# Kernel tuning notes

Hardware: AMD Instinct MI355X
Metric: run time of the kernel (lower is better)

Reference implementation:

```python
import jax, jax.numpy as jnp
import numpy as np

VOCAB, EMB, HID, B, S = 32000, 512, 512, 64, 1024


def setup_inputs() -> dict:
    key = jax.random.key(0)
    ks = jax.random.split(key, 9)
    x = jax.random.randint(ks[0], (B, S), 0, VOCAB)
    lengths = jax.random.randint(ks[1], (B,), 1, S + 1)
    # embedding table; padding_idx=0 row is zero-initialized in torch
    emb_table = jax.random.normal(ks[2], (VOCAB, EMB), dtype=jnp.float32) * 0.02
    emb_table = emb_table.at[0].set(0.0)
    sc_e = 1.0 / np.sqrt(EMB)
    sc_h = 1.0 / np.sqrt(HID)
    W_ih0 = jax.random.uniform(ks[3], (EMB, HID), jnp.float32, -sc_e, sc_e)
    b0 = jax.random.uniform(ks[4], (HID,), jnp.float32, -sc_e, sc_e)
    W_hh0 = jax.random.uniform(ks[5], (HID, HID), jnp.float32, -sc_h, sc_h)
    W_ih1 = jax.random.uniform(ks[6], (HID, HID), jnp.float32, -sc_h, sc_h)
    b1 = jax.random.uniform(ks[7], (HID,), jnp.float32, -sc_h, sc_h)
    W_hh1 = jax.random.uniform(ks[8], (HID, HID), jnp.float32, -sc_h, sc_h)
    return {"x": x, "lengths": lengths, "emb_table": emb_table,
            "W_ih0": W_ih0, "b0": b0, "W_hh0": W_hh0,
            "W_ih1": W_ih1, "b1": b1, "W_hh1": W_hh1}


def reference(x, lengths, emb_table, W_ih0, b0, W_hh0, W_ih1, b1, W_hh1):
    # eval mode: dropout is identity
    emb = emb_table[x]                    # [B, S, E]
    emb_t = jnp.transpose(emb, (1, 0, 2))  # [S, B, E] for scan over time
    h0_init = jnp.zeros((x.shape[0], HID), emb.dtype)
    h1_init = jnp.zeros((x.shape[0], HID), emb.dtype)

    def step(carry, x_t):
        h0, h1 = carry
        h0 = jnp.tanh(x_t @ W_ih0 + b0 + h0 @ W_hh0)
        h1 = jnp.tanh(h0 @ W_ih1 + b1 + h1 @ W_hh1)
        return (h0, h1), h1

    (h0, h1), outs = jax.lax.scan(step, (h0_init, h1_init), emb_t)
    outputs = jnp.transpose(outs, (1, 0, 2))   # [B, S, H]
    hidden = jnp.stack([h0, h1], axis=0)       # [num_layers, B, H]
    return outputs, hidden
```

## Files before the change

kernel.cpp:

```cpp
#include <hip/hip_runtime.h>

#define S_LEN 1024
#define BATCH 64
#define HIDDEN 512
#define NGROUP 4
#define NBLK 32
#define COLS_PER_BLK 16
#define GRID_CAND 512
#define TRY_CAP (1 << 20)

typedef __attribute__((ext_vector_type(8))) short short8;
typedef __attribute__((ext_vector_type(4))) float f32x4;
typedef __attribute__((ext_vector_type(4))) unsigned int u32x4;

__device__ __forceinline__ unsigned short f2bf(float x) {
  unsigned u = __builtin_bit_cast(unsigned, x);
  u += 0x7fffu + ((u >> 16) & 1u);
  return (unsigned short)(u >> 16);
}
__device__ __forceinline__ float bf2f(unsigned short h) {
  unsigned u = ((unsigned)h) << 16;
  return __builtin_bit_cast(float, u);
}

#define HOFF(p, kc, l) ((((p) * 16 + (kc)) * 64 + (l)) * 8)

__global__ void k_init(unsigned* __restrict__ ws, int* __restrict__ hbufs) {
  int i = blockIdx.x * blockDim.x + threadIdx.x;
  if (i < 4096) ws[i] = 0u;
  for (int k = i; k < 131072; k += gridDim.x * blockDim.x) hbufs[k] = 0;
}

__launch_bounds__(256, 1)
__global__ void k_rnn(const int* __restrict__ x, const float* __restrict__ emb,
                      const float* __restrict__ Wih0, const float* __restrict__ b0,
                      const float* __restrict__ Whh0, const float* __restrict__ Wih1,
                      const float* __restrict__ b1, const float* __restrict__ Whh1,
                      float* __restrict__ out, unsigned* __restrict__ ws_u,
                      short* __restrict__ hbase) {
  __shared__ short wlds[8 * 16 * 64 * 8];
  __shared__ __align__(16) short stage0[2][32][8];
  __shared__ __align__(16) short stage1[2][32][8];
  __shared__ float accx[3][8][68];
  __shared__ int slot_sh, grp_sh;

  if (threadIdx.x == 0) {
    unsigned xcc;
    asm volatile("s_getreg_b32 %0, hwreg(HW_REG_XCC_ID)" : "=s"(xcc));
    int s = -1;
    if (xcc < NGROUP)
      s = (int)__hip_atomic_fetch_add(ws_u + 2048 + xcc * 16, 1u,
                                      __ATOMIC_RELAXED, __HIP_MEMORY_SCOPE_AGENT);
    slot_sh = s; grp_sh = (int)xcc;
  }
  __syncthreads();
  const int slot = slot_sh, grp = grp_sh;
  if ((unsigned)slot >= NBLK) return;

  const int tid  = threadIdx.x;
  const int wid  = tid >> 6;
  const int lane = tid & 63;
  const int col0 = slot * COLS_PER_BLK;

  {
    const float* Wm[4] = {Wih0, Whh0, Wih1, Whh1};
    const int c = col0 + (lane & 15);
    #pragma unroll
    for (int m = 0; m < 4; ++m) {
      const float* W = Wm[m];
      for (int kc = wid; kc < 16; kc += 4) {
        const int k0 = kc * 32 + (lane >> 4) * 8;
        const int basei = (kc * 64 + lane) * 8;
        #pragma unroll
        for (int j = 0; j < 8; ++j) {
          float v = W[(size_t)(k0 + j) * HIDDEN + c];
          unsigned short vh = f2bf(v);
          wlds[(m * 2    ) * 8192 + basei + j] = (short)vh;
          wlds[(m * 2 + 1) * 8192 + basei + j] = (short)f2bf(v - bf2f(vh));
        }
      }
    }
  }
  __syncthreads();

  short* gh    = hbase + grp * 65536;
  short* h0_hi = gh;
  short* h0_lo = gh + 16384;
  short* h1_hi = gh + 32768;
  short* h1_lo = gh + 49152;

  const int row0  = grp * 16;
  const int arow  = row0 + (lane & 15);
  const int kgo   = (lane >> 4) * 8;
  const int ccol  = col0 + (lane & 15);
  const int drow0 = (lane >> 4) * 4;
  const float bc0 = b0[ccol];
  const float bc1 = b1[ccol];

  const int skc   = col0 >> 5;
  const int sub0  = (slot & 1) * 2;
  const int sel2  = (lane & 15) >> 3;
  const int sjj   = lane & 7;

  float* out_seq = out;
  float* hidden  = out + (size_t)BATCH * S_LEN * HIDDEN;

  unsigned* gflags = ws_u + grp * 512;
  unsigned*       myflag = gflags + slot * 16;
  const unsigned* pollp  = gflags + (lane & 31) * 16;

  short8 ea_reg[4];
  #define LOAD_EA(t) do {                                                   \
    const int xr_ = x[arow * S_LEN + (t)];                                  \
    const float* erow_ = emb + (size_t)xr_ * HIDDEN;                        \
    _Pragma("unroll")                                                       \
    for (int k2 = 0; k2 < 4; ++k2) {                                        \
      const float4* ep_ = (const float4*)(erow_ + (wid * 4 + k2) * 32 + kgo); \
      float4 e0_ = ep_[0], e1_ = ep_[1];                                    \
      short8 ea_;                                                           \
      ea_[0] = (short)f2bf(e0_.x); ea_[1] = (short)f2bf(e0_.y);             \
      ea_[2] = (short)f2bf(e0_.z); ea_[3] = (short)f2bf(e0_.w);             \
      ea_[4] = (short)f2bf(e1_.x); ea_[5] = (short)f2bf(e1_.y);             \
      ea_[6] = (short)f2bf(e1_.z); ea_[7] = (short)f2bf(e1_.w);             \
      ea_reg[k2] = ea_;                                                     \
    } } while (0)

  LOAD_EA(0);

  for (int i = 0; i <= S_LEN; ++i) {
    const int p = i & 1;
    const int q = p ^ 1;
    const bool doL0 = (i < S_LEN);
    const bool doL1 = (i >= 1);

    f32x4 aA0 = {0.f, 0.f, 0.f, 0.f};
    f32x4 aA1 = {0.f, 0.f, 0.f, 0.f};
    f32x4 aB0 = {0.f, 0.f, 0.f, 0.f};
    f32x4 aB1 = {0.f, 0.f, 0.f, 0.f};
    #pragma unroll
    for (int k2 = 0; k2 < 4; ++k2) {
      const int kc = wid * 4 + k2;
      const int o0 = HOFF(q, kc, lane);
      const int o1 = HOFF(p, kc, lane);
      short8 ah = *(const short8*)(h0_hi + o0);
      short8 al = *(const short8*)(h0_lo + o0);
      short8 ch = *(const short8*)(h1_hi + o1);
      short8 cl = *(const short8*)(h1_lo + o1);
      const int fb = (kc * 64 + lane) * 8;
      if (doL0) {
        short8 w0h = *(const short8*)&wlds[0 * 8192 + fb];
        short8 w0l = *(const short8*)&wlds[1 * 8192 + fb];
        short8 g0h = *(const short8*)&wlds[2 * 8192 + fb];
        short8 g0l = *(const short8*)&wlds[3 * 8192 + fb];
        f32x4& ac = (k2 & 1) ? aA1 : aA0;
        ac = __builtin_amdgcn_mfma_f32_16x16x32_bf16(ea_reg[k2], w0h, ac, 0, 0, 0);
        ac = __builtin_amdgcn_mfma_f32_16x16x32_bf16(ea_reg[k2], w0l, ac, 0, 0, 0);
        ac = __builtin_amdgcn_mfma_f32_16x16x32_bf16(ah, g0h, ac, 0, 0, 0);
        ac = __builtin_amdgcn_mfma_f32_16x16x32_bf16(ah, g0l, ac, 0, 0, 0);
        ac = __builtin_amdgcn_mfma_f32_16x16x32_bf16(al, g0h, ac, 0, 0, 0);
      }
      if (doL1) {
        short8 w1h = *(const short8*)&wlds[4 * 8192 + fb];
        short8 w1l = *(const short8*)&wlds[5 * 8192 + fb];
        short8 g1h = *(const short8*)&wlds[6 * 8192 + fb];
        short8 g1l = *(const short8*)&wlds[7 * 8192 + fb];
        f32x4& bcx = (k2 & 1) ? aB1 : aB0;
        bcx = __builtin_amdgcn_mfma_f32_16x16x32_bf16(ah, w1h, bcx, 0, 0, 0);
        bcx = __builtin_amdgcn_mfma_f32_16x16x32_bf16(ah, w1l, bcx, 0, 0, 0);
        bcx = __builtin_amdgcn_mfma_f32_16x16x32_bf16(al, w1h, bcx, 0, 0, 0);
        bcx = __builtin_amdgcn_mfma_f32_16x16x32_bf16(ch, g1h, bcx, 0, 0, 0);
        bcx = __builtin_amdgcn_mfma_f32_16x16x32_bf16(ch, g1l, bcx, 0, 0, 0);
        bcx = __builtin_amdgcn_mfma_f32_16x16x32_bf16(cl, g1h, bcx, 0, 0, 0);
      }
    }

    if (wid) {
      #pragma unroll
      for (int j = 0; j < 4; ++j) {
        accx[wid - 1][j    ][lane] = aA0[j] + aA1[j];
        accx[wid - 1][4 + j][lane] = aB0[j] + aB1[j];
      }
    }
    __syncthreads();

    if (wid == 0) {
      float hv0[4], hv1[4];
      if (doL0) {
        #pragma unroll
        for (int j = 0; j < 4; ++j) {
          float s = aA0[j] + aA1[j] + accx[0][j][lane] + accx[1][j][lane]
                  + accx[2][j][lane] + bc0;
          hv0[j] = tanhf(s);
          unsigned short hi = f2bf(hv0[j]);
          unsigned short lo = f2bf(hv0[j] - bf2f(hi));
          stage0[0][drow0 + j + 16 * sel2][sjj] = (short)hi;
          stage0[1][drow0 + j + 16 * sel2][sjj] = (short)lo;
        }
      }
      if (doL1) {
        #pragma unroll
        for (int j = 0; j < 4; ++j) {
          float s = aB0[j] + aB1[j] + accx[0][4 + j][lane] + accx[1][4 + j][lane]
                  + accx[2][4 + j][lane] + bc1;
          hv1[j] = tanhf(s);
          unsigned short hi = f2bf(hv1[j]);
          unsigned short lo = f2bf(hv1[j] - bf2f(hi));
          stage1[0][drow0 + j + 16 * sel2][sjj] = (short)hi;
          stage1[1][drow0 + j + 16 * sel2][sjj] = (short)lo;
        }
      }
      asm volatile("s_waitcnt lgkmcnt(0)" ::: "memory");
      const int l2 = lane & 31, sel = lane >> 5;
      if (doL0) {
        u32x4 v = *(const u32x4*)&stage0[sel][l2][0];
        short* dst = (sel ? h0_lo : h0_hi) + HOFF(p, skc, sub0 * 16 + l2);
        *(u32x4*)dst = v;
      }
      if (doL1) {
        u32x4 v = *(const u32x4*)&stage1[sel][l2][0];
        short* dst = (sel ? h1_lo : h1_hi) + HOFF(q, skc, sub0 * 16 + l2);
        *(u32x4*)dst = v;
      }
      if (doL1) {
        const int t = i - 1;
        #pragma unroll
        for (int j = 0; j < 4; ++j)
          out_seq[(size_t)(row0 + drow0 + j) * S_LEN * HIDDEN
                  + (size_t)t * HIDDEN + ccol] = hv1[j];
        if (i == S_LEN) {
          #pragma unroll
          for (int j = 0; j < 4; ++j)
            hidden[32768 + (row0 + drow0 + j) * HIDDEN + ccol] = hv1[j];
        }
      }
      if (doL0 && i == S_LEN - 1) {
        #pragma unroll
        for (int j = 0; j < 4; ++j)
          hidden[(row0 + drow0 + j) * HIDDEN + ccol] = hv0[j];
      }
    }

    if (i < S_LEN) {
      if (wid == 0) {
        asm volatile("s_waitcnt vmcnt(0)" ::: "memory");
        if (lane == 0)
          __hip_atomic_store(myflag, (unsigned)(i + 1),
                             __ATOMIC_RELAXED, __HIP_MEMORY_SCOPE_AGENT);
      }
      if (i + 1 < S_LEN) LOAD_EA(i + 1);
      __builtin_amdgcn_sched_barrier(0);
      if (wid == 0) {
        int tries = 0;
        for (;;) {
          unsigned f = __hip_atomic_load(pollp, __ATOMIC_RELAXED,
                                         __HIP_MEMORY_SCOPE_AGENT);
          if (__all((int)(f > (unsigned)i))) break;
          if (++tries > TRY_CAP) break;
        }
      }
      __syncthreads();
    }
  }
  #undef LOAD_EA
}

extern "C" void kernel_launch(void* const* d_in, const int* in_sizes, int n_in,
                              void* d_out, int out_size, void* d_ws, size_t ws_size,
                              hipStream_t stream) {
  const int*   x    = (const int*)d_in[0];
  const float* emb  = (const float*)d_in[2];
  const float* Wih0 = (const float*)d_in[3];
  const float* b0   = (const float*)d_in[4];
  const float* Whh0 = (const float*)d_in[5];
  const float* Wih1 = (const float*)d_in[6];
  const float* b1   = (const float*)d_in[7];
  const float* Whh1 = (const float*)d_in[8];
  float* out = (float*)d_out;

  unsigned* ws_u  = (unsigned*)d_ws;
  short*    hbase = (short*)((char*)d_ws + 16384);

  k_init<<<256, 256, 0, stream>>>(ws_u, (int*)hbase);
  k_rnn<<<GRID_CAND, 256, 0, stream>>>(x, emb, Wih0, b0, Whh0, Wih1, b1, Whh1,
                                       out, ws_u, hbase);
}
```

Baseline: 3.602 ms.

## Offload output stores and embedding prefetch from wave 0 to wave 1

Takes the output-sequence and final-hidden global stores, plus wave 0's embedding prefetch, off the critical wave 0. Wave 1 now recomputes the tanh results from shared partial sums and handles those stores. It also loads wave 0's embedding fragments and hands them over through shared memory after the barrier. Wave 0 raises its priority while finishing the step and signalling the flag, which shortens the serial per-step path. The cost is extra shared-memory traffic, duplicated tanh work in wave 1 and an extra LDS read for wave 0 after the sync.

```diff
diff --git a/kernel.cpp b/kernel.cpp
--- a/kernel.cpp
+++ b/kernel.cpp
@@ -41,7 +41,8 @@
   __shared__ short wlds[8 * 16 * 64 * 8];
   __shared__ __align__(16) short stage0[2][32][8];
   __shared__ __align__(16) short stage1[2][32][8];
-  __shared__ float accx[3][8][68];
+  __shared__ float accx[4][8][68];
+  __shared__ __align__(16) short eastage[4][64][8];
   __shared__ int slot_sh, grp_sh;
 
   if (threadIdx.x == 0) {
@@ -110,6 +111,14 @@
   const unsigned* pollp  = gflags + (lane & 31) * 16;
 
   short8 ea_reg[4];
+  #define CVT_EA(e0_, e1_, dst_) do {                                       \
+    short8 ea_;                                                             \
+    ea_[0] = (short)f2bf(e0_.x); ea_[1] = (short)f2bf(e0_.y);               \
+    ea_[2] = (short)f2bf(e0_.z); ea_[3] = (short)f2bf(e0_.w);               \
+    ea_[4] = (short)f2bf(e1_.x); ea_[5] = (short)f2bf(e1_.y);               \
+    ea_[6] = (short)f2bf(e1_.z); ea_[7] = (short)f2bf(e1_.w);               \
+    dst_ = ea_; } while (0)
+
   #define LOAD_EA(t) do {                                                   \
     const int xr_ = x[arow * S_LEN + (t)];                                  \
     const float* erow_ = emb + (size_t)xr_ * HIDDEN;                        \
@@ -117,12 +126,22 @@
     for (int k2 = 0; k2 < 4; ++k2) {                                        \
       const float4* ep_ = (const float4*)(erow_ + (wid * 4 + k2) * 32 + kgo); \
       float4 e0_ = ep_[0], e1_ = ep_[1];                                    \
-      short8 ea_;                                                           \
-      ea_[0] = (short)f2bf(e0_.x); ea_[1] = (short)f2bf(e0_.y);             \
-      ea_[2] = (short)f2bf(e0_.z); ea_[3] = (short)f2bf(e0_.w);             \
-      ea_[4] = (short)f2bf(e1_.x); ea_[5] = (short)f2bf(e1_.y);             \
-      ea_[6] = (short)f2bf(e1_.z); ea_[7] = (short)f2bf(e1_.w);             \
-      ea_reg[k2] = ea_;                                                     \
+      CVT_EA(e0_, e1_, ea_reg[k2]);                                         \
+    } } while (0)
+
+  #define LOAD_EA2(t) do {                                                  \
+    const int xr_ = x[arow * S_LEN + (t)];                                  \
+    const float* erow_ = emb + (size_t)xr_ * HIDDEN;                        \
+    _Pragma("unroll")                                                       \
+    for (int k2 = 0; k2 < 4; ++k2) {                                        \
+      const float4* e0p_ = (const float4*)(erow_ + k2 * 32 + kgo);          \
+      const float4* e1p_ = (const float4*)(erow_ + (4 + k2) * 32 + kgo);    \
+      float4 a0_ = e0p_[0], a1_ = e0p_[1];                                  \
+      float4 b0_ = e1p_[0], b1_ = e1p_[1];                                  \
+      short8 w0frag_;                                                       \
+      CVT_EA(a0_, a1_, w0frag_);                                            \
+      *(short8*)&eastage[k2][lane][0] = w0frag_;                            \
+      CVT_EA(b0_, b1_, ea_reg[k2]);                                         \
     } } while (0)
 
   LOAD_EA(0);
@@ -174,25 +193,26 @@
       }
     }
 
-    if (wid) {
-      #pragma unroll
-      for (int j = 0; j < 4; ++j) {
-        accx[wid - 1][j    ][lane] = aA0[j] + aA1[j];
-        accx[wid - 1][4 + j][lane] = aB0[j] + aB1[j];
-      }
+    #pragma unroll
+    for (int j = 0; j < 4; ++j) {
+      accx[wid][j    ][lane] = aA0[j] + aA1[j];
+      accx[wid][4 + j][lane] = aB0[j] + aB1[j];
     }
     __syncthreads();
 
+    #define FINAL0(j) tanhf(accx[0][(j)][lane] + accx[1][(j)][lane] + \
+                            accx[2][(j)][lane] + accx[3][(j)][lane] + bc0)
+    #define FINAL1(j) tanhf(accx[0][4+(j)][lane] + accx[1][4+(j)][lane] + \
+                            accx[2][4+(j)][lane] + accx[3][4+(j)][lane] + bc1)
+
     if (wid == 0) {
-      float hv0[4], hv1[4];
+      __builtin_amdgcn_s_setprio(1);
       if (doL0) {
         #pragma unroll
         for (int j = 0; j < 4; ++j) {
-          float s = aA0[j] + aA1[j] + accx[0][j][lane] + accx[1][j][lane]
-                  + accx[2][j][lane] + bc0;
-          hv0[j] = tanhf(s);
-          unsigned short hi = f2bf(hv0[j]);
-          unsigned short lo = f2bf(hv0[j] - bf2f(hi));
+          float hv = FINAL0(j);
+          unsigned short hi = f2bf(hv);
+          unsigned short lo = f2bf(hv - bf2f(hi));
           stage0[0][drow0 + j + 16 * sel2][sjj] = (short)hi;
           stage0[1][drow0 + j + 16 * sel2][sjj] = (short)lo;
         }
@@ -200,11 +220,9 @@
       if (doL1) {
         #pragma unroll
         for (int j = 0; j < 4; ++j) {
-          float s = aB0[j] + aB1[j] + accx[0][4 + j][lane] + accx[1][4 + j][lane]
-                  + accx[2][4 + j][lane] + bc1;
-          hv1[j] = tanhf(s);
-          unsigned short hi = f2bf(hv1[j]);
-          unsigned short lo = f2bf(hv1[j] - bf2f(hi));
+          float hv = FINAL1(j);
+          unsigned short hi = f2bf(hv);
+          unsigned short lo = f2bf(hv - bf2f(hi));
           stage1[0][drow0 + j + 16 * sel2][sjj] = (short)hi;
           stage1[1][drow0 + j + 16 * sel2][sjj] = (short)lo;
         }
@@ -221,33 +239,38 @@
         short* dst = (sel ? h1_lo : h1_hi) + HOFF(q, skc, sub0 * 16 + l2);
         *(u32x4*)dst = v;
       }
-      if (doL1) {
-        const int t = i - 1;
-        #pragma unroll
-        for (int j = 0; j < 4; ++j)
-          out_seq[(size_t)(row0 + drow0 + j) * S_LEN * HIDDEN
-                  + (size_t)t * HIDDEN + ccol] = hv1[j];
-        if (i == S_LEN) {
-          #pragma unroll
-          for (int j = 0; j < 4; ++j)
-            hidden[32768 + (row0 + drow0 + j) * HIDDEN + ccol] = hv1[j];
-        }
-      }
-      if (doL0 && i == S_LEN - 1) {
-        #pragma unroll
-        for (int j = 0; j < 4; ++j)
-          hidden[(row0 + drow0 + j) * HIDDEN + ccol] = hv0[j];
-      }
-    }
-
-    if (i < S_LEN) {
-      if (wid == 0) {
+      if (i < S_LEN) {
         asm volatile("s_waitcnt vmcnt(0)" ::: "memory");
         if (lane == 0)
           __hip_atomic_store(myflag, (unsigned)(i + 1),
                              __ATOMIC_RELAXED, __HIP_MEMORY_SCOPE_AGENT);
       }
+      __builtin_amdgcn_s_setprio(0);
+    } else if (wid == 1) {
+      if (doL1) {
+        const int t = i - 1;
+        #pragma unroll
+        for (int j = 0; j < 4; ++j) {
+          float hv = FINAL1(j);
+          out_seq[(size_t)(row0 + drow0 + j) * S_LEN * HIDDEN
+                  + (size_t)t * HIDDEN + ccol] = hv;
+          if (i == S_LEN)
+            hidden[32768 + (row0 + drow0 + j) * HIDDEN + ccol] = hv;
+        }
+      }
+      if (doL0 && i == S_LEN - 1) {
+        #pragma unroll
+        for (int j = 0; j < 4; ++j)
+          hidden[(row0 + drow0 + j) * HIDDEN + ccol] = FINAL0(j);
+      }
+      if (i + 1 < S_LEN) LOAD_EA2(i + 1);
+    } else {
       if (i + 1 < S_LEN) LOAD_EA(i + 1);
+    }
+    #undef FINAL0
+    #undef FINAL1
+
+    if (i < S_LEN) {
       __builtin_amdgcn_sched_barrier(0);
       if (wid == 0) {
         int tries = 0;
@@ -259,9 +282,16 @@
         }
       }
       __syncthreads();
+      if (wid == 0 && i + 1 < S_LEN) {
+        #pragma unroll
+        for (int k2 = 0; k2 < 4; ++k2)
+          ea_reg[k2] = *(const short8*)&eastage[k2][lane][0];
+      }
     }
   }
   #undef LOAD_EA
+  #undef LOAD_EA2
+  #undef CVT_EA
 }
 
 extern "C" void kernel_launch(void* const* d_in, const int* in_sizes, int n_in,
```

New measurement: 3.892 ms. 8.1% more time.
